# Optimization experiments

Measured on AMD Instinct MI355X. Metric: run time of the kernel, lower is better.

## Reference

```python
import jax, jax.numpy as jnp
import numpy as np
import itertools

N_BOX = 19
B = 2048
T = 5
_EDGES = np.array(list(itertools.combinations(range(N_BOX), 2)))  # [E,2], E=171
ROW = jnp.asarray(_EDGES[:, 0])
COL = jnp.asarray(_EDGES[:, 1])


def setup_inputs() -> dict:
    key = jax.random.key(0)
    ks = jax.random.split(key, 8)
    return {
        "location_t": jax.random.uniform(ks[0], (B, N_BOX, 5), dtype=jnp.float32),
        "feature_t": jax.random.normal(ks[1], (B, N_BOX, 512), dtype=jnp.float32),
        "mask_t": jax.random.randint(ks[2], (B, N_BOX), 0, 2).astype(bool),
        "past_location_t": jax.random.uniform(ks[3], (B, T, N_BOX, 6), dtype=jnp.float32),
        "W1": jax.random.normal(ks[4], (512, 256), dtype=jnp.float32) * 0.05,
        "b1": jax.random.normal(ks[5], (256,), dtype=jnp.float32) * 0.05,
        "W2": jax.random.normal(ks[6], (256, 512), dtype=jnp.float32) * 0.05,
        "b2": jax.random.normal(ks[7], (512,), dtype=jnp.float32) * 0.05,
    }


def _edge_weights(location_t, mask, past_location_t):
    # bbox centers from cols 1..4: [B,N]
    cx = 0.5 * (location_t[:, :, 1] + location_t[:, :, 3])
    cy = 0.5 * (location_t[:, :, 2] + location_t[:, :, 4])
    d = (cx[:, ROW] - cx[:, COL]) ** 2 + (cy[:, ROW] - cy[:, COL]) ** 2  # [B,E]

    # motion distance, vectorized over all nodes then gathered per edge
    cp = past_location_t[:, :, :, 3:-1] - past_location_t[:, :, :, 1:3]  # [B,T,N,2]
    cpx = cp[..., 0] * 1280.0  # [B,T,N]
    cpy = cp[..., 1] * 720.0
    dx = cpx[:, -1] - cpx[:, 0]  # [B,N]
    dy = cpy[:, -1] - cpy[:, 0]
    length = jnp.sqrt(dx ** 2 + dy ** 2)
    length = jnp.where(length == 0.0, 1.0, length)
    ndx = dx / length
    ndy = dy / length
    x0 = cpx[:, 0]  # [B,N]
    y0 = cpy[:, 0]
    d1 = jnp.sqrt((x0[:, ROW] + ndx[:, ROW] - x0[:, COL] - ndx[:, COL]) ** 2
                  + (y0[:, ROW] + ndy[:, ROW] - y0[:, COL] - ndy[:, COL]) ** 2)
    d2 = jnp.sqrt((x0[:, ROW] - x0[:, COL]) ** 2 + (y0[:, ROW] - y0[:, COL]) ** 2)
    md = d1 - d2  # [B,E]

    w = jnp.exp(-(0.7 * d + 0.3 * md))
    valid = mask[:, ROW] & mask[:, COL]
    w = jnp.where(valid, w, 0.0)
    wmin = jnp.min(w, axis=1, keepdims=True)
    wmax = jnp.max(w, axis=1, keepdims=True)
    return (w - wmin) / (wmax - wmin)


def _gcn(x, ew, W, b):
    # PyG GCNConv: add self loops (weight 1), symmetric normalization, x@W, scatter-add, +bias
    n = x.shape[0]
    loops = jnp.arange(n)
    row = jnp.concatenate([ROW, loops])
    col = jnp.concatenate([COL, loops])
    ew_full = jnp.concatenate([ew, jnp.ones((n,), ew.dtype)])
    deg = jax.ops.segment_sum(ew_full, col, num_segments=n)
    dinv = jnp.where(deg > 0, deg ** -0.5, 0.0)
    norm = dinv[row] * ew_full * dinv[col]  # [E+N]
    xw = x @ W  # [N,F_out]
    out = jnp.zeros((n, W.shape[1]), xw.dtype).at[col].add(norm[:, None] * xw[row])
    return out + b


def reference(location_t, feature_t, mask_t, past_location_t, W1, b1, W2, b2):
    w = _edge_weights(location_t, mask_t, past_location_t)  # [B,E]

    def per_graph(x, ew):
        h = jax.nn.sigmoid(_gcn(x, ew, W1, b1))
        return jax.nn.sigmoid(_gcn(h, ew, W2, b2))

    return jax.vmap(per_graph)(feature_t, w)  # [B,19,512]
```

## Files before the change

kernel.cpp:

```cpp
#include <hip/hip_runtime.h>
#include <hip/hip_bf16.h>
#include <math.h>

#define NBOX 19
#define NEDGE 171
#define TT 5
#define BATCH 2048
#define GB 2
#define MR (GB * NBOX)
#define MP 48

typedef __attribute__((ext_vector_type(8))) short short8v;
typedef __attribute__((ext_vector_type(4))) float f32x4;

static __device__ __forceinline__ ushort f2bf(float f) {
    __hip_bfloat16 h = __float2bfloat16(f);
    return *reinterpret_cast<ushort*>(&h);
}

__device__ __forceinline__ int edge_index(int r, int c) {
    return r * (NBOX - 1) - (r * (r - 1)) / 2 + (c - r - 1);
}

__global__ __launch_bounds__(192) void adjbf_kernel(
    const float* __restrict__ loc,
    const int*   __restrict__ mask,
    const float* __restrict__ past,
    ushort* __restrict__ adjbf)
{
    int b = blockIdx.x;
    int tid = threadIdx.x;
    __shared__ float cx[NBOX], cy[NBOX], x0[NBOX], y0[NBOX], ndx[NBOX], ndy[NBOX];
    __shared__ int   mv[NBOX];
    __shared__ float w[NEDGE];
    __shared__ float dinv[NBOX];
    __shared__ float wmin_s, wmax_s;

    if (tid < NBOX) {
        const float* l = loc + ((size_t)b * NBOX + tid) * 5;
        cx[tid] = 0.5f * (l[1] + l[3]);
        cy[tid] = 0.5f * (l[2] + l[4]);
        const float* p0 = past + (((size_t)b * TT + 0) * NBOX + tid) * 6;
        const float* p4 = past + (((size_t)b * TT + (TT - 1)) * NBOX + tid) * 6;
        float cpx0 = (p0[3] - p0[1]) * 1280.0f, cpy0 = (p0[4] - p0[2]) * 720.0f;
        float cpx4 = (p4[3] - p4[1]) * 1280.0f, cpy4 = (p4[4] - p4[2]) * 720.0f;
        float dx = cpx4 - cpx0, dy = cpy4 - cpy0;
        float len = sqrtf(dx * dx + dy * dy);
        if (len == 0.0f) len = 1.0f;
        ndx[tid] = dx / len;
        ndy[tid] = dy / len;
        x0[tid] = cpx0;
        y0[tid] = cpy0;
        mv[tid] = mask[(size_t)b * NBOX + tid];
    }
    __syncthreads();

    float wv = 0.0f;
    if (tid < NEDGE) {
        int rem = tid, rr = 0;
        while (rem >= NBOX - 1 - rr) { rem -= NBOX - 1 - rr; rr++; }
        int r = rr, c = rr + 1 + rem;
        float ddx = cx[r] - cx[c], ddy = cy[r] - cy[c];
        float d = ddx * ddx + ddy * ddy;
        float ax = x0[r] + ndx[r] - x0[c] - ndx[c];
        float ay = y0[r] + ndy[r] - y0[c] - ndy[c];
        float d1 = sqrtf(ax * ax + ay * ay);
        float bx = x0[r] - x0[c], by = y0[r] - y0[c];
        float d2 = sqrtf(bx * bx + by * by);
        float md = d1 - d2;
        wv = expf(-(0.7f * d + 0.3f * md));
        if (!(mv[r] && mv[c])) wv = 0.0f;
        w[tid] = wv;
    }
    __syncthreads();

    if (tid == 0) {
        float mn = w[0], mx = w[0];
        for (int i = 1; i < NEDGE; i++) { mn = fminf(mn, w[i]); mx = fmaxf(mx, w[i]); }
        wmin_s = mn; wmax_s = mx;
    }
    __syncthreads();

    float inv_range = 1.0f / (wmax_s - wmin_s);
    if (tid < NEDGE) w[tid] = (wv - wmin_s) * inv_range;
    __syncthreads();

    if (tid < NBOX) {
        float s = 1.0f;
        for (int rr = 0; rr < tid; rr++) s += w[edge_index(rr, tid)];
        dinv[tid] = 1.0f / sqrtf(s);
    }
    __syncthreads();

    ushort* A = adjbf + (size_t)b * 1024;
    for (int idx = tid; idx < 1024; idx += 192) {
        int r = idx & 31, cc = idx >> 5;
        float v = 0.0f;
        if (r < NBOX && cc < NBOX) {
            if (r == cc) v = dinv[r] * dinv[r];
            else if (r < cc) v = w[edge_index(r, cc)] * dinv[r] * dinv[cc];
        }
        A[idx] = f2bf(v);
    }
}

__global__ void packT_kernel(const float* __restrict__ src, ushort* __restrict__ dst,
                             int K, int N)
{
    int total = K * N;
    for (int idx = blockIdx.x * blockDim.x + threadIdx.x; idx < total;
         idx += gridDim.x * blockDim.x) {
        int n = idx / K, k = idx % K;
        dst[idx] = f2bf(src[(size_t)k * N + n]);
    }
}

__global__ __launch_bounds__(256, 4) void fused_kernel(
    const float*  __restrict__ feat,
    const ushort* __restrict__ adjbf,
    const ushort* __restrict__ W1T,
    const ushort* __restrict__ W2T,
    const float*  __restrict__ b1,
    const float*  __restrict__ b2,
    float* __restrict__ out)
{
    __shared__ __align__(16) ushort XHs[MP * 256];
    __shared__ __align__(16) ushort YsT[64 * 64];
    __shared__ __align__(16) ushort AdjS[MP * 64];

    const int tid = threadIdx.x;
    const int lane = tid & 63, wv = tid >> 6;
    const int rowbase = blockIdx.x * MR;
    const int bbase = blockIdx.x * GB;
    const int ncol = wv * 16 + (lane & 15);
    const int kgrp = lane >> 4;
    const int l15 = lane & 15;

#pragma unroll
    for (int p = 0; p < 2; p++)
        ((int4*)YsT)[tid + p * 256] = make_int4(0, 0, 0, 0);

    for (int i = tid; i < MP * 64; i += 256) {
        int row = i >> 6, col = i & 63;
        ushort v = 0;
        if (row < MR) {
            int g = (row >= NBOX) ? 1 : 0;
            int cc = row - g * NBOX;
            int rc = col - g * NBOX;
            if ((unsigned)rc < (unsigned)NBOX)
                v = adjbf[(size_t)(bbase + g) * 1024 + cc * 32 + rc];
        }
        int boff = (row * 128 + col * 2) ^ ((row & 7) << 4);
        *(ushort*)((char*)AdjS + boff) = v;
    }

    f32x4 acc1[4][3];
#pragma unroll
    for (int c = 0; c < 4; c++)
#pragma unroll
        for (int m = 0; m < 3; m++) acc1[c][m] = (f32x4){0.f, 0.f, 0.f, 0.f};

    for (int kh = 0; kh < 2; kh++) {
        __syncthreads();
        const float* fg = feat + (size_t)rowbase * 512 + kh * 256;
#pragma unroll
        for (int p = 0; p < 12; p++) {
            int i = tid + p * 256;
            int row = i >> 6, q = i & 63;
            ushort4 h;
            if (i < MR * 64) {
                float4 v = *(const float4*)(fg + (size_t)row * 512 + q * 4);
                h.x = f2bf(v.x); h.y = f2bf(v.y); h.z = f2bf(v.z); h.w = f2bf(v.w);
            } else {
                h.x = 0; h.y = 0; h.z = 0; h.w = 0;
            }
            int boff = (row * 512 + q * 8) ^ ((row & 7) << 4);
            *(ushort4*)((char*)XHs + boff) = h;
        }
        __syncthreads();

        const ushort* bpb = W1T + (size_t)ncol * 512 + kh * 256 + kgrp * 8;
        short8v bcur[4], bnxt[4];
#pragma unroll
        for (int c = 0; c < 4; c++)
            bcur[c] = *(const short8v*)(bpb + (size_t)c * 64 * 512);
#pragma unroll
        for (int ks = 0; ks < 8; ks++) {
            if (ks < 7) {
#pragma unroll
                for (int c = 0; c < 4; c++)
                    bnxt[c] = *(const short8v*)(bpb + (size_t)c * 64 * 512 + (ks + 1) * 32);
            }
            short8v a[3];
#pragma unroll
            for (int m = 0; m < 3; m++) {
                int row = m * 16 + l15;
                int boff = (row * 512 + ks * 64 + kgrp * 16) ^ ((row & 7) << 4);
                a[m] = *(const short8v*)((char*)XHs + boff);
            }
#pragma unroll
            for (int c = 0; c < 4; c++)
#pragma unroll
                for (int m = 0; m < 3; m++)
                    acc1[c][m] = __builtin_amdgcn_mfma_f32_16x16x32_bf16(
                        a[m], bcur[c], acc1[c][m], 0, 0, 0);
#pragma unroll
            for (int c = 0; c < 4; c++) bcur[c] = bnxt[c];
        }
    }

#pragma unroll
    for (int c = 0; c < 4; c++) {
        __syncthreads();
#pragma unroll
        for (int m = 0; m < 3; m++) {
            int gr0 = m * 16 + kgrp * 4;
            ushort4 hq;
            hq.x = f2bf(acc1[c][m][0]); hq.y = f2bf(acc1[c][m][1]);
            hq.z = f2bf(acc1[c][m][2]); hq.w = f2bf(acc1[c][m][3]);
            int boff = (ncol * 128 + gr0 * 2) ^ ((ncol & 7) << 4);
            *(ushort4*)((char*)YsT + boff) = hq;
        }
        __syncthreads();
        short8v yb[2];
#pragma unroll
        for (int ks = 0; ks < 2; ks++)
            yb[ks] = *(const short8v*)((char*)YsT +
                     ((ncol * 128 + ks * 64 + kgrp * 16) ^ ((ncol & 7) << 4)));
        float bv = b1[c * 64 + ncol];
#pragma unroll
        for (int mt = 0; mt < 3; mt++) {
            f32x4 o = (f32x4){0.f, 0.f, 0.f, 0.f};
#pragma unroll
            for (int ks = 0; ks < 2; ks++) {
                int ar = mt * 16 + l15;
                short8v af = *(const short8v*)((char*)AdjS +
                             ((ar * 128 + ks * 64 + kgrp * 16) ^ ((ar & 7) << 4)));
                o = __builtin_amdgcn_mfma_f32_16x16x32_bf16(af, yb[ks], o, 0, 0, 0);
            }
#pragma unroll
            for (int j = 0; j < 4; j++) {
                int grp = mt * 16 + kgrp * 4 + j;
                float s = 1.0f / (1.0f + expf(-(o[j] + bv)));
                int boff = (grp * 512 + (c * 64 + ncol) * 2) ^ ((grp & 7) << 4);
                *(ushort*)((char*)XHs + boff) = f2bf(s);
            }
        }
    }
    __syncthreads();

#pragma unroll 1
    for (int half = 0; half < 2; half++) {
        f32x4 acc[4][3];
#pragma unroll
        for (int c = 0; c < 4; c++)
#pragma unroll
            for (int m = 0; m < 3; m++) acc[c][m] = (f32x4){0.f, 0.f, 0.f, 0.f};

        const ushort* bpb = W2T + (size_t)(half * 256 + ncol) * 256 + kgrp * 8;
        short8v bcur[4], bnxt[4];
#pragma unroll
        for (int c = 0; c < 4; c++)
            bcur[c] = *(const short8v*)(bpb + (size_t)c * 64 * 256);
#pragma unroll
        for (int ks = 0; ks < 8; ks++) {
            if (ks < 7) {
#pragma unroll
                for (int c = 0; c < 4; c++)
                    bnxt[c] = *(const short8v*)(bpb + (size_t)c * 64 * 256 + (ks + 1) * 32);
            }
            short8v a[3];
#pragma unroll
            for (int m = 0; m < 3; m++) {
                int row = m * 16 + l15;
                int boff = (row * 512 + ks * 64 + kgrp * 16) ^ ((row & 7) << 4);
                a[m] = *(const short8v*)((char*)XHs + boff);
            }
#pragma unroll
            for (int c = 0; c < 4; c++)
#pragma unroll
                for (int m = 0; m < 3; m++)
                    acc[c][m] = __builtin_amdgcn_mfma_f32_16x16x32_bf16(
                        a[m], bcur[c], acc[c][m], 0, 0, 0);
#pragma unroll
            for (int c = 0; c < 4; c++) bcur[c] = bnxt[c];
        }

#pragma unroll
        for (int c = 0; c < 4; c++) {
            int cg = half * 4 + c;
            __syncthreads();
#pragma unroll
            for (int m = 0; m < 3; m++) {
                int gr0 = m * 16 + kgrp * 4;
                ushort4 hq;
                hq.x = f2bf(acc[c][m][0]); hq.y = f2bf(acc[c][m][1]);
                hq.z = f2bf(acc[c][m][2]); hq.w = f2bf(acc[c][m][3]);
                int boff = (ncol * 128 + gr0 * 2) ^ ((ncol & 7) << 4);
                *(ushort4*)((char*)YsT + boff) = hq;
            }
            __syncthreads();
            short8v yb[2];
#pragma unroll
            for (int ks = 0; ks < 2; ks++)
                yb[ks] = *(const short8v*)((char*)YsT +
                         ((ncol * 128 + ks * 64 + kgrp * 16) ^ ((ncol & 7) << 4)));
            float bv = b2[cg * 64 + ncol];
#pragma unroll
            for (int mt = 0; mt < 3; mt++) {
                f32x4 o = (f32x4){0.f, 0.f, 0.f, 0.f};
#pragma unroll
                for (int ks = 0; ks < 2; ks++) {
                    int ar = mt * 16 + l15;
                    short8v af = *(const short8v*)((char*)AdjS +
                                 ((ar * 128 + ks * 64 + kgrp * 16) ^ ((ar & 7) << 4)));
                    o = __builtin_amdgcn_mfma_f32_16x16x32_bf16(af, yb[ks], o, 0, 0, 0);
                }
#pragma unroll
                for (int j = 0; j < 4; j++) {
                    int grp = mt * 16 + kgrp * 4 + j;
                    if (grp < MR) {
                        float s = 1.0f / (1.0f + expf(-(o[j] + bv)));
                        out[(size_t)(rowbase + grp) * 512 + cg * 64 + ncol] = s;
                    }
                }
            }
        }
    }
}

extern "C" void kernel_launch(void* const* d_in, const int* in_sizes, int n_in,
                              void* d_out, int out_size, void* d_ws, size_t ws_size,
                              hipStream_t stream) {
    const float* loc  = (const float*)d_in[0];
    const float* feat = (const float*)d_in[1];
    const int*   mask = (const int*)d_in[2];
    const float* past = (const float*)d_in[3];
    const float* W1   = (const float*)d_in[4];
    const float* b1   = (const float*)d_in[5];
    const float* W2   = (const float*)d_in[6];
    const float* b2   = (const float*)d_in[7];

    ushort* adjbf = (ushort*)d_ws;
    ushort* W1T   = adjbf + (size_t)BATCH * 1024;
    ushort* W2T   = W1T + 256 * 512;

    adjbf_kernel<<<BATCH, 192, 0, stream>>>(loc, mask, past, adjbf);
    packT_kernel<<<512, 256, 0, stream>>>(W1, W1T, 512, 256);
    packT_kernel<<<256, 256, 0, stream>>>(W2, W2T, 256, 512);

    fused_kernel<<<BATCH / GB, 256, 0, stream>>>(feat, adjbf, W1T, W2T, b1, b2,
                                                 (float*)d_out);
}
```

Before: 120.9 us.

## Drop per-column barriers, deepen weight prefetch, use fast sigmoid and bf16 convert

Removes the two __syncthreads around each per-column-group YsT staging step, since each wave only writes and reads its own YsT rows. One barrier is kept after the layer-1 GEMM so no wave overwrites XHs while another is still reading it. Weight-fragment prefetch goes from double to triple buffering (two k-steps ahead), replacing the register copy at the end of each step. Sigmoid now uses __expf plus a hardware reciprocal, and float-to-bf16 conversion uses a round-half-up bit trick with no NaN handling, which trades some accuracy and edge-case correctness for fewer instructions.

After: 110.3 us. 8.8% less time.

```diff
diff --git a/kernel.cpp b/kernel.cpp
--- a/kernel.cpp
+++ b/kernel.cpp
@@ -14,8 +14,12 @@
 typedef __attribute__((ext_vector_type(4))) float f32x4;
 
 static __device__ __forceinline__ ushort f2bf(float f) {
-    __hip_bfloat16 h = __float2bfloat16(f);
-    return *reinterpret_cast<ushort*>(&h);
+    unsigned int u = __builtin_bit_cast(unsigned int, f);
+    return (ushort)((u + 0x8000u) >> 16);
+}
+
+static __device__ __forceinline__ float sigm(float x) {
+    return __builtin_amdgcn_rcpf(1.0f + __expf(-x));
 }
 
 __device__ __forceinline__ int edge_index(int r, int c) {
@@ -129,10 +133,10 @@
     __shared__ __align__(16) ushort AdjS[MP * 64];
 
     const int tid = threadIdx.x;
-    const int lane = tid & 63, wv = tid >> 6;
+    const int lane = tid & 63, wvi = tid >> 6;
     const int rowbase = blockIdx.x * MR;
     const int bbase = blockIdx.x * GB;
-    const int ncol = wv * 16 + (lane & 15);
+    const int ncol = wvi * 16 + (lane & 15);
     const int kgrp = lane >> 4;
     const int l15 = lane & 15;
 
@@ -180,16 +184,20 @@
         __syncthreads();
 
         const ushort* bpb = W1T + (size_t)ncol * 512 + kh * 256 + kgrp * 8;
-        short8v bcur[4], bnxt[4];
-#pragma unroll
-        for (int c = 0; c < 4; c++)
-            bcur[c] = *(const short8v*)(bpb + (size_t)c * 64 * 512);
+        short8v br[3][4];
+#pragma unroll
+        for (int c = 0; c < 4; c++)
+            br[0][c] = *(const short8v*)(bpb + (size_t)c * 64 * 512);
+#pragma unroll
+        for (int c = 0; c < 4; c++)
+            br[1][c] = *(const short8v*)(bpb + (size_t)c * 64 * 512 + 32);
 #pragma unroll
         for (int ks = 0; ks < 8; ks++) {
-            if (ks < 7) {
+            if (ks < 6) {
 #pragma unroll
                 for (int c = 0; c < 4; c++)
-                    bnxt[c] = *(const short8v*)(bpb + (size_t)c * 64 * 512 + (ks + 1) * 32);
+                    br[(ks + 2) % 3][c] =
+                        *(const short8v*)(bpb + (size_t)c * 64 * 512 + (ks + 2) * 32);
             }
             short8v a[3];
 #pragma unroll
@@ -203,15 +211,13 @@
 #pragma unroll
                 for (int m = 0; m < 3; m++)
                     acc1[c][m] = __builtin_amdgcn_mfma_f32_16x16x32_bf16(
-                        a[m], bcur[c], acc1[c][m], 0, 0, 0);
-#pragma unroll
-            for (int c = 0; c < 4; c++) bcur[c] = bnxt[c];
-        }
-    }
+                        a[m], br[ks % 3][c], acc1[c][m], 0, 0, 0);
+        }
+    }
+    __syncthreads();
 
 #pragma unroll
     for (int c = 0; c < 4; c++) {
-        __syncthreads();
 #pragma unroll
         for (int m = 0; m < 3; m++) {
             int gr0 = m * 16 + kgrp * 4;
@@ -221,7 +227,6 @@
             int boff = (ncol * 128 + gr0 * 2) ^ ((ncol & 7) << 4);
             *(ushort4*)((char*)YsT + boff) = hq;
         }
-        __syncthreads();
         short8v yb[2];
 #pragma unroll
         for (int ks = 0; ks < 2; ks++)
@@ -241,7 +246,7 @@
 #pragma unroll
             for (int j = 0; j < 4; j++) {
                 int grp = mt * 16 + kgrp * 4 + j;
-                float s = 1.0f / (1.0f + expf(-(o[j] + bv)));
+                float s = sigm(o[j] + bv);
                 int boff = (grp * 512 + (c * 64 + ncol) * 2) ^ ((grp & 7) << 4);
                 *(ushort*)((char*)XHs + boff) = f2bf(s);
             }
@@ -258,16 +263,20 @@
             for (int m = 0; m < 3; m++) acc[c][m] = (f32x4){0.f, 0.f, 0.f, 0.f};
 
         const ushort* bpb = W2T + (size_t)(half * 256 + ncol) * 256 + kgrp * 8;
-        short8v bcur[4], bnxt[4];
-#pragma unroll
-        for (int c = 0; c < 4; c++)
-            bcur[c] = *(const short8v*)(bpb + (size_t)c * 64 * 256);
+        short8v br[3][4];
+#pragma unroll
+        for (int c = 0; c < 4; c++)
+            br[0][c] = *(const short8v*)(bpb + (size_t)c * 64 * 256);
+#pragma unroll
+        for (int c = 0; c < 4; c++)
+            br[1][c] = *(const short8v*)(bpb + (size_t)c * 64 * 256 + 32);
 #pragma unroll
         for (int ks = 0; ks < 8; ks++) {
-            if (ks < 7) {
+            if (ks < 6) {
 #pragma unroll
                 for (int c = 0; c < 4; c++)
-                    bnxt[c] = *(const short8v*)(bpb + (size_t)c * 64 * 256 + (ks + 1) * 32);
+                    br[(ks + 2) % 3][c] =
+                        *(const short8v*)(bpb + (size_t)c * 64 * 256 + (ks + 2) * 32);
             }
             short8v a[3];
 #pragma unroll
@@ -281,15 +290,12 @@
 #pragma unroll
                 for (int m = 0; m < 3; m++)
                     acc[c][m] = __builtin_amdgcn_mfma_f32_16x16x32_bf16(
-                        a[m], bcur[c], acc[c][m], 0, 0, 0);
-#pragma unroll
-            for (int c = 0; c < 4; c++) bcur[c] = bnxt[c];
+                        a[m], br[ks % 3][c], acc[c][m], 0, 0, 0);
         }
 
 #pragma unroll
         for (int c = 0; c < 4; c++) {
             int cg = half * 4 + c;
-            __syncthreads();
 #pragma unroll
             for (int m = 0; m < 3; m++) {
                 int gr0 = m * 16 + kgrp * 4;
@@ -299,7 +305,6 @@
                 int boff = (ncol * 128 + gr0 * 2) ^ ((ncol & 7) << 4);
                 *(ushort4*)((char*)YsT + boff) = hq;
             }
-            __syncthreads();
             short8v yb[2];
 #pragma unroll
             for (int ks = 0; ks < 2; ks++)
@@ -320,7 +325,7 @@
                 for (int j = 0; j < 4; j++) {
                     int grp = mt * 16 + kgrp * 4 + j;
                     if (grp < MR) {
-                        float s = 1.0f / (1.0f + expf(-(o[j] + bv)));
+                        float s = sigm(o[j] + bv);
                         out[(size_t)(rowbase + grp) * 512 + cg * 64 + ncol] = s;
                     }
                 }
```
